# Performance work log

Hardware: AMD Instinct MI355X
Metric: run time of the kernel (lower is better)

## Reference

```python
import jax, jax.numpy as jnp
import numpy as np

HID = 1024
HEADS = 16
HEAD_DIM = HID // HEADS
FFN = 4096
EPS = 1e-5


def setup_inputs() -> dict:
    key = jax.random.key(0)
    ks = jax.random.split(key, 12)
    s = lambda k, shape, fan_in: jax.random.normal(k, shape, jnp.float32) * (fan_in ** -0.5)
    return {
        "hidden_states": jax.random.normal(ks[0], (2, 2048, HID), jnp.float32),
        "Wq": s(ks[1], (HID, HID), HID),
        "Wk": s(ks[2], (HID, HID), HID),
        "Wv": s(ks[3], (HID, HID), HID),
        "Wo": s(ks[4], (HID, HID), HID),
        "W1": s(ks[5], (HID, FFN), HID),
        "b1": jnp.zeros((FFN,), jnp.float32),
        "W2": s(ks[6], (FFN, HID), FFN),
        "b2": jnp.zeros((HID,), jnp.float32),
        "ln1_scale": jnp.ones((HID,), jnp.float32),
        "ln1_shift": jnp.zeros((HID,), jnp.float32),
        "ln2_scale": jnp.ones((HID,), jnp.float32),
        "ln2_shift": jnp.zeros((HID,), jnp.float32),
    }


def _layer_norm(x, scale, shift):
    mean = jnp.mean(x, axis=-1, keepdims=True)
    var = jnp.var(x, axis=-1, keepdims=True)  # biased, matches unbiased=False
    return (x - mean) * jax.lax.rsqrt(var + EPS) * scale + shift


def _forward(hidden_states, Wq, Wk, Wv, Wo, W1, b1, W2, b2,
             ln1_scale, ln1_shift, ln2_scale, ln2_shift):
    bsz, seq_len, _ = hidden_states.shape
    residual = hidden_states
    x = _layer_norm(hidden_states, ln1_scale, ln1_shift)

    # q/k/v projections -> [b, h, s, d]
    def proj(W):
        return (x @ W).reshape(bsz, seq_len, HEADS, HEAD_DIM).transpose(0, 2, 1, 3)
    q, k, v = proj(Wq), proj(Wk), proj(Wv)

    scores = jnp.einsum("bhqd,bhkd->bhqk", q, k)
    causal = jnp.triu(jnp.ones((seq_len, seq_len), bool), k=1)
    scores = jnp.where(causal, -jnp.inf, scores) / (HEAD_DIM ** 0.5)
    attn = jax.nn.softmax(scores, axis=-1)  # dropout is identity in eval
    out = jnp.einsum("bhqk,bhkd->bhqd", attn, v)
    out = out.transpose(0, 2, 1, 3).reshape(bsz, seq_len, HID)
    hidden_states = residual + out @ Wo

    residual = hidden_states
    y = _layer_norm(hidden_states, ln2_scale, ln2_shift)
    y = jax.nn.gelu(y @ W1 + b1, approximate=False) @ W2 + b2  # torch nn.GELU default = exact erf
    return residual + y


def reference(hidden_states, Wq, Wk, Wv, Wo, W1, b1, W2, b2,
              ln1_scale, ln1_shift, ln2_scale, ln2_shift):
    return _forward(hidden_states, Wq, Wk, Wv, Wo, W1, b1, W2, b2,
                    ln1_scale, ln1_shift, ln2_scale, ln2_shift)
```

## Files before the change

kernel.cpp:

```cpp
#include <hip/hip_runtime.h>
#include <math.h>

using bf16x8 = __attribute__((ext_vector_type(8))) short;
using f32x4  = __attribute__((ext_vector_type(4))) float;

struct __align__(8) us4 { unsigned short x, y, z, w; };

__device__ __forceinline__ unsigned short f2b(float f) {
  union { float f; unsigned u; } v; v.f = f;
  unsigned r = v.u + 0x7FFFu + ((v.u >> 16) & 1u);
  return (unsigned short)(r >> 16);
}

#define GLDS(g, l) __builtin_amdgcn_global_load_lds(                        \
    (const __attribute__((address_space(1))) void*)(g),                    \
    (__attribute__((address_space(3))) void*)(l), 16, 0, 0)

__global__ void __launch_bounds__(256) transpose_w(
    const float* __restrict__ src, unsigned short* __restrict__ dst,
    int K, int N) {
  __shared__ float tile[32][33];
  const int n0 = blockIdx.x * 32, k0 = blockIdx.y * 32;
  const int tx = threadIdx.x & 31, ty = threadIdx.x >> 5;
#pragma unroll
  for (int i = 0; i < 32; i += 8)
    tile[ty + i][tx] = src[(size_t)(k0 + ty + i) * N + n0 + tx];
  __syncthreads();
#pragma unroll
  for (int i = 0; i < 32; i += 8)
    dst[(size_t)(n0 + ty + i) * K + k0 + tx] = f2b(tile[tx][ty + i]);
}

__global__ void __launch_bounds__(256) ln_kernel(
    const float* __restrict__ in, const float* __restrict__ scale,
    const float* __restrict__ shift, unsigned short* __restrict__ out) {
  const int row = blockIdx.x, t = threadIdx.x;
  const float4 v = ((const float4*)(in + (size_t)row * 1024))[t];
  float s  = v.x + v.y + v.z + v.w;
  float s2 = v.x * v.x + v.y * v.y + v.z * v.z + v.w * v.w;
#pragma unroll
  for (int off = 32; off; off >>= 1) {
    s  += __shfl_xor(s,  off);
    s2 += __shfl_xor(s2, off);
  }
  __shared__ float red[8];
  const int w = t >> 6, lane = t & 63;
  if (!lane) { red[w] = s; red[4 + w] = s2; }
  __syncthreads();
  s  = red[0] + red[1] + red[2] + red[3];
  s2 = red[4] + red[5] + red[6] + red[7];
  const float mean = s * (1.0f / 1024.0f);
  const float var  = s2 * (1.0f / 1024.0f) - mean * mean;
  const float rstd = rsqrtf(var + 1e-5f);
  const float4 sc = ((const float4*)scale)[t];
  const float4 sh = ((const float4*)shift)[t];
  us4 o;
  o.x = f2b((v.x - mean) * rstd * sc.x + sh.x);
  o.y = f2b((v.y - mean) * rstd * sc.y + sh.y);
  o.z = f2b((v.z - mean) * rstd * sc.z + sh.z);
  o.w = f2b((v.w - mean) * rstd * sc.w + sh.w);
  ((us4*)(out + (size_t)row * 1024))[t] = o;
}

template <int MODE, int BM>
__global__ void __launch_bounds__(256) gemm_bt(
    const unsigned short* __restrict__ A, const unsigned short* __restrict__ B,
    int K, int N,
    float* __restrict__ outf, unsigned short* __restrict__ outb,
    const float* __restrict__ bias, const float* __restrict__ resid,
    unsigned short* __restrict__ vt) {
  constexpr int WN = (BM == 128) ? 2 : 4;
  constexpr int NJ = 128 / (16 * WN);
  constexpr int ACH = BM / 32;
  __shared__ unsigned short lA[2][BM * 64];
  __shared__ unsigned short lB[2][128 * 64];
  const int t = threadIdx.x, lane = t & 63;
  const int w = t >> 6, wm = w / WN, wn = w % WN;
  const int r16 = lane & 15, g = lane >> 4;
  const int m0 = blockIdx.x * BM, n0 = blockIdx.y * 128;

  const unsigned short* aSrc[ACH];
  const unsigned short* bSrc[4];
#pragma unroll
  for (int p = 0; p < ACH; ++p) {
    const int ci = t + p * 256, m = ci >> 3, cs = ci & 7;
    aSrc[p] = A + (size_t)(m0 + m) * K + (cs ^ (m & 7)) * 8;
  }
#pragma unroll
  for (int p = 0; p < 4; ++p) {
    const int ci = t + p * 256, m = ci >> 3, cs = ci & 7;
    bSrc[p] = B + (size_t)(n0 + m) * K + (cs ^ (m & 7)) * 8;
  }

  int aOff[4][2], bOff[NJ][2];
#pragma unroll
  for (int i = 0; i < 4; ++i)
#pragma unroll
    for (int ks = 0; ks < 2; ++ks) {
      const int m = wm * 64 + i * 16 + r16, kb = ks * 4 + g;
      aOff[i][ks] = ((m << 3) + (kb ^ (m & 7))) << 3;
    }
#pragma unroll
  for (int j = 0; j < NJ; ++j)
#pragma unroll
    for (int ks = 0; ks < 2; ++ks) {
      const int n = wn * (16 * NJ) + j * 16 + r16, kb = ks * 4 + g;
      bOff[j][ks] = ((n << 3) + (kb ^ (n & 7))) << 3;
    }

  auto stage = [&](int buf, int kt) {
    const int off = kt * 64;
#pragma unroll
    for (int p = 0; p < ACH; ++p)
      GLDS(aSrc[p] + off, &lA[buf][(t + p * 256) * 8]);
#pragma unroll
    for (int p = 0; p < 4; ++p)
      GLDS(bSrc[p] + off, &lB[buf][(t + p * 256) * 8]);
  };

  f32x4 acc[4][NJ] = {};
  const int nkt = K >> 6;
  stage(0, 0);
  __syncthreads();
  for (int kt = 0; kt < nkt; ++kt) {
    const int cur = kt & 1;
    if (kt + 1 < nkt) stage(cur ^ 1, kt + 1);
    const unsigned short* bA = lA[cur];
    const unsigned short* bB = lB[cur];
#pragma unroll
    for (int ks = 0; ks < 2; ++ks) {
      bf16x8 af[4], bfr[NJ];
#pragma unroll
      for (int i = 0; i < 4; ++i) af[i] = *(const bf16x8*)&bA[aOff[i][ks]];
#pragma unroll
      for (int j = 0; j < NJ; ++j) bfr[j] = *(const bf16x8*)&bB[bOff[j][ks]];
#pragma unroll
      for (int i = 0; i < 4; ++i)
#pragma unroll
        for (int j = 0; j < NJ; ++j)
          acc[i][j] = __builtin_amdgcn_mfma_f32_16x16x32_bf16(
              af[i], bfr[j], acc[i][j], 0, 0, 0);
    }
    __syncthreads();
  }

  float bj[NJ];
  if constexpr (MODE == 2 || MODE == 3) {
#pragma unroll
    for (int j = 0; j < NJ; ++j)
      bj[j] = bias[n0 + wn * (16 * NJ) + j * 16 + r16];
  }
#pragma unroll
  for (int i = 0; i < 4; ++i) {
    const int row0 = m0 + wm * 64 + i * 16 + g * 4;
#pragma unroll
    for (int j = 0; j < NJ; ++j) {
      const int colb = n0 + wn * (16 * NJ) + j * 16;
      const int col = colb + r16;
      if constexpr (MODE == 0) {
        if (colb < 2048) {
#pragma unroll
          for (int r = 0; r < 4; ++r)
            outb[(size_t)(row0 + r) * 2048 + col] = f2b(acc[i][j][r]);
        } else {
          const int b = row0 >> 11, s0 = row0 & 2047;
          us4 pk;
          pk.x = f2b(acc[i][j][0]); pk.y = f2b(acc[i][j][1]);
          pk.z = f2b(acc[i][j][2]); pk.w = f2b(acc[i][j][3]);
          *(us4*)&vt[((size_t)b * 1024 + (col - 2048)) * 2048 + s0] = pk;
        }
      } else if constexpr (MODE == 1) {
#pragma unroll
        for (int r = 0; r < 4; ++r) {
          const size_t idx = (size_t)(row0 + r) * N + col;
          outf[idx] = acc[i][j][r] + resid[idx];
        }
      } else if constexpr (MODE == 2) {
#pragma unroll
        for (int r = 0; r < 4; ++r) {
          const float x = acc[i][j][r] + bj[j];
          const float u = x * (0.7978845608028654f + 0.03567740814f * x * x);
          const float e = __builtin_amdgcn_exp2f(u * 2.885390081777927f);
          const float th = 1.0f - 2.0f * __builtin_amdgcn_rcpf(e + 1.0f);
          outb[(size_t)(row0 + r) * N + col] = f2b(0.5f * x * (1.0f + th));
        }
      } else {
#pragma unroll
        for (int r = 0; r < 4; ++r) {
          const size_t idx = (size_t)(row0 + r) * N + col;
          outf[idx] = acc[i][j][r] + bj[j] + resid[idx];
        }
      }
    }
  }
}

__global__ void __launch_bounds__(256) attn_kernel(
    const unsigned short* __restrict__ qk, const unsigned short* __restrict__ vt,
    unsigned short* __restrict__ obuf) {
  const int j = blockIdx.x, h = blockIdx.y, bb = blockIdx.z;
  const int t = threadIdx.x, lane = t & 63, w = t >> 6;
  const int r16 = lane & 15, g = lane >> 4;
  __shared__ unsigned short lK[2][64 * 64];
  __shared__ unsigned short lV[2][64 * 64];
  __shared__ unsigned short lP[4][16 * 72];

  const int qtA = j, qtB = 31 - j;
  const int ktmax = qtB;
  const int qrowA = qtA * 64 + w * 16 + r16;
  const int qrowB = qtB * 64 + w * 16 + r16;
  const float CE = 0.18033688011112042f;

  bf16x8 qfA[2], qfB[2];
  {
    const unsigned short* qa =
        qk + (size_t)(bb * 2048 + qrowA) * 2048 + h * 64;
    qfA[0] = *(const bf16x8*)(qa + g * 8);
    qfA[1] = *(const bf16x8*)(qa + 32 + g * 8);
    const unsigned short* qb =
        qk + (size_t)(bb * 2048 + qrowB) * 2048 + h * 64;
    qfB[0] = *(const bf16x8*)(qb + g * 8);
    qfB[1] = *(const bf16x8*)(qb + 32 + g * 8);
  }

  f32x4 accA[4] = {}, accB[4] = {};
  float mA = -3.0e38f, lA_ = 0.0f, mB = -3.0e38f, lB_ = 0.0f;

  auto stage = [&](int buf, int kt) {
    const int k0 = kt * 64;
#pragma unroll
    for (int p = 0; p < 2; ++p) {
      const int ci = t + p * 256;
      const int r = ci >> 3, cs = ci & 7;
      const int cb = cs ^ (r & 7);
      GLDS(qk + (size_t)(bb * 2048 + k0 + r) * 2048 + 1024 + h * 64 + cb * 8,
           &lK[buf][ci * 8]);
      GLDS(vt + ((size_t)bb * 1024 + h * 64 + r) * 2048 + k0 + cb * 8,
           &lV[buf][ci * 8]);
    }
  };

  auto flash_step = [&](const bf16x8* qf, f32x4* accO, float& mrun,
                        float& lrun, int qrow, bool diag, int k0, int cur) {
    f32x4 s[4] = {};
#pragma unroll
    for (int ks = 0; ks < 2; ++ks)
#pragma unroll
      for (int mt = 0; mt < 4; ++mt) {
        const int r = mt * 16 + r16, db = ks * 4 + g;
        const bf16x8 kf =
            *(const bf16x8*)&lK[cur][((r << 3) + (db ^ (r & 7))) << 3];
        s[mt] = __builtin_amdgcn_mfma_f32_16x16x32_bf16(kf, qf[ks], s[mt],
                                                        0, 0, 0);
      }
    if (diag) {
#pragma unroll
      for (int mt = 0; mt < 4; ++mt)
#pragma unroll
        for (int r = 0; r < 4; ++r)
          if (k0 + mt * 16 + g * 4 + r > qrow) s[mt][r] = -3.0e38f;
    }
    float tmax = -3.0e38f;
#pragma unroll
    for (int mt = 0; mt < 4; ++mt)
#pragma unroll
      for (int r = 0; r < 4; ++r) tmax = fmaxf(tmax, s[mt][r]);
    tmax = fmaxf(tmax, __shfl_xor(tmax, 16));
    tmax = fmaxf(tmax, __shfl_xor(tmax, 32));
    const float mnew = fmaxf(mrun, tmax);
    const float fac = __builtin_amdgcn_exp2f((mrun - mnew) * CE);
    float pv[4][4];
    float tsum = 0.0f;
#pragma unroll
    for (int mt = 0; mt < 4; ++mt)
#pragma unroll
      for (int r = 0; r < 4; ++r) {
        pv[mt][r] = __builtin_amdgcn_exp2f((s[mt][r] - mnew) * CE);
        tsum += pv[mt][r];
      }
    tsum += __shfl_xor(tsum, 16);
    tsum += __shfl_xor(tsum, 32);
    lrun = lrun * fac + tsum;
    mrun = mnew;
#pragma unroll
    for (int mt = 0; mt < 4; ++mt) {
      us4 pk;
      pk.x = f2b(pv[mt][0]); pk.y = f2b(pv[mt][1]);
      pk.z = f2b(pv[mt][2]); pk.w = f2b(pv[mt][3]);
      *(us4*)&lP[w][r16 * 72 + mt * 16 + g * 4] = pk;
    }
    float fr[4];
#pragma unroll
    for (int r = 0; r < 4; ++r) fr[r] = __shfl(fac, g * 4 + r);
#pragma unroll
    for (int nb = 0; nb < 4; ++nb)
#pragma unroll
      for (int r = 0; r < 4; ++r) accO[nb][r] *= fr[r];
#pragma unroll
    for (int ks = 0; ks < 2; ++ks) {
      const bf16x8 pa = *(const bf16x8*)&lP[w][r16 * 72 + ks * 32 + g * 8];
#pragma unroll
      for (int nb = 0; nb < 4; ++nb) {
        const int d = nb * 16 + r16, kb = ks * 4 + g;
        const bf16x8 vf =
            *(const bf16x8*)&lV[cur][((d << 3) + (kb ^ (d & 7))) << 3];
        accO[nb] = __builtin_amdgcn_mfma_f32_16x16x32_bf16(pa, vf, accO[nb],
                                                           0, 0, 0);
      }
    }
  };

  stage(0, 0);
  __syncthreads();
  int cur = 0;
  for (int kt = 0; kt <= ktmax; ++kt) {
    if (kt < ktmax) stage(cur ^ 1, kt + 1);
    flash_step(qfB, accB, mB, lB_, qrowB, kt == qtB, kt * 64, cur);
    if (kt <= qtA)
      flash_step(qfA, accA, mA, lA_, qrowA, kt == qtA, kt * 64, cur);
    __syncthreads();
    cur ^= 1;
  }

  auto epilogue = [&](const f32x4* accO, float lrun, int q0) {
    const float li = 1.0f / lrun;
    float lr_[4];
#pragma unroll
    for (int r = 0; r < 4; ++r) lr_[r] = __shfl(li, g * 4 + r);
#pragma unroll
    for (int nb = 0; nb < 4; ++nb)
#pragma unroll
      for (int r = 0; r < 4; ++r) {
        const int row = bb * 2048 + q0 + w * 16 + g * 4 + r;
        const int col = h * 64 + nb * 16 + r16;
        obuf[(size_t)row * 1024 + col] = f2b(accO[nb][r] * lr_[r]);
      }
  };
  epilogue(accA, lA_, qtA * 64);
  epilogue(accB, lB_, qtB * 64);
}

extern "C" void kernel_launch(void* const* d_in, const int* in_sizes, int n_in,
                              void* d_out, int out_size, void* d_ws,
                              size_t ws_size, hipStream_t stream) {
  const float* hs   = (const float*)d_in[0];
  const float* Wq   = (const float*)d_in[1];
  const float* Wk   = (const float*)d_in[2];
  const float* Wv   = (const float*)d_in[3];
  const float* Wo   = (const float*)d_in[4];
  const float* W1   = (const float*)d_in[5];
  const float* b1   = (const float*)d_in[6];
  const float* W2   = (const float*)d_in[7];
  const float* b2   = (const float*)d_in[8];
  const float* ln1s = (const float*)d_in[9];
  const float* ln1b = (const float*)d_in[10];
  const float* ln2s = (const float*)d_in[11];
  const float* ln2b = (const float*)d_in[12];
  float* out = (float*)d_out;

  char* ws = (char*)d_ws;
  unsigned short* wqkvT = (unsigned short*)(ws + 0);
  unsigned short* woT   = (unsigned short*)(ws + 6291456);
  unsigned short* w1T   = (unsigned short*)(ws + 8388608);
  unsigned short* w2T   = (unsigned short*)(ws + 16777216);
  float*          hid   = (float*)(ws + 25165824);
  unsigned short* xb    = (unsigned short*)(ws + 41943040);
  char*           big   = ws + 50331648;
  unsigned short* qkb   = (unsigned short*)(big);
  unsigned short* vtb   = (unsigned short*)(big + 16777216);
  unsigned short* ob    = (unsigned short*)(big + 25165824);
  unsigned short* h1    = (unsigned short*)(big);

  transpose_w<<<dim3(32, 32), 256, 0, stream>>>(Wq, wqkvT, 1024, 1024);
  transpose_w<<<dim3(32, 32), 256, 0, stream>>>(Wk, wqkvT + 1024 * 1024, 1024, 1024);
  transpose_w<<<dim3(32, 32), 256, 0, stream>>>(Wv, wqkvT + 2 * 1024 * 1024, 1024, 1024);
  transpose_w<<<dim3(32, 32), 256, 0, stream>>>(Wo, woT, 1024, 1024);
  transpose_w<<<dim3(128, 32), 256, 0, stream>>>(W1, w1T, 1024, 4096);
  transpose_w<<<dim3(32, 128), 256, 0, stream>>>(W2, w2T, 4096, 1024);

  ln_kernel<<<4096, 256, 0, stream>>>(hs, ln1s, ln1b, xb);
  gemm_bt<0, 128><<<dim3(32, 24), 256, 0, stream>>>(xb, wqkvT, 1024, 3072,
                                                    nullptr, qkb, nullptr, nullptr, vtb);
  attn_kernel<<<dim3(16, 16, 2), 256, 0, stream>>>(qkb, vtb, ob);
  gemm_bt<1, 64><<<dim3(64, 8), 256, 0, stream>>>(ob, woT, 1024, 1024,
                                                  hid, nullptr, nullptr, hs, nullptr);
  ln_kernel<<<4096, 256, 0, stream>>>(hid, ln2s, ln2b, xb);
  gemm_bt<2, 128><<<dim3(32, 32), 256, 0, stream>>>(xb, w1T, 1024, 4096,
                                                    nullptr, h1, b1, nullptr, nullptr);
  gemm_bt<3, 64><<<dim3(64, 8), 256, 0, stream>>>(h1, w2T, 4096, 1024,
                                                  out, nullptr, b2, hid, nullptr);
}
```

Baseline: 245.1 us.

## Split attention KV range across two blocks and merge partial softmax results

Each attention block's causal KV range is split into two halves, doubling the grid to 1024 blocks. Each half writes unnormalized bf16 partial outputs plus running max and sum, and a new merge kernel combines them with log-sum-exp weights. The aim is better CU occupancy and load balance, since 512 blocks underfill the GPU. It also adds lazy rescaling (skip the rescale when the max barely grows), packed bf16 conversion via v_cvt_pk_bf16_f32, an XOR-swizzled P buffer, and s_setprio around the MFMAs. The costs are an extra launch, extra global traffic for the partials, and some precision loss from storing partials in bf16.

Result: slower. 257.7 us (+5.1%).

```diff
diff --git a/kernel.cpp b/kernel.cpp
--- a/kernel.cpp
+++ b/kernel.cpp
@@ -5,11 +5,21 @@
 using f32x4  = __attribute__((ext_vector_type(4))) float;
 
 struct __align__(8) us4 { unsigned short x, y, z, w; };
+struct __align__(8) u32x2 { unsigned int x, y; };
 
 __device__ __forceinline__ unsigned short f2b(float f) {
   union { float f; unsigned u; } v; v.f = f;
   unsigned r = v.u + 0x7FFFu + ((v.u >> 16) & 1u);
   return (unsigned short)(r >> 16);
+}
+__device__ __forceinline__ float b2f(unsigned short b) {
+  union { unsigned u; float f; } v; v.u = ((unsigned)b) << 16;
+  return v.f;
+}
+__device__ __forceinline__ unsigned int cvt_pk_bf16(float lo, float hi) {
+  unsigned int d;
+  asm("v_cvt_pk_bf16_f32 %0, %1, %2" : "=v"(d) : "v"(lo), "v"(hi));
+  return d;
 }
 
 #define GLDS(g, l) __builtin_amdgcn_global_load_lds(                        \
@@ -197,28 +207,33 @@
 
 __global__ void __launch_bounds__(256) attn_kernel(
     const unsigned short* __restrict__ qk, const unsigned short* __restrict__ vt,
-    unsigned short* __restrict__ obuf) {
-  const int j = blockIdx.x, h = blockIdx.y, bb = blockIdx.z;
+    unsigned short* __restrict__ Op, float* __restrict__ mlm,
+    float* __restrict__ mll) {
+  const int j = blockIdx.x, h = blockIdx.y;
+  const int bb = blockIdx.z >> 1, half = blockIdx.z & 1;
   const int t = threadIdx.x, lane = t & 63, w = t >> 6;
   const int r16 = lane & 15, g = lane >> 4;
   __shared__ unsigned short lK[2][64 * 64];
   __shared__ unsigned short lV[2][64 * 64];
-  __shared__ unsigned short lP[4][16 * 72];
+  __shared__ unsigned short lP[4][16 * 64];
 
   const int qtA = j, qtB = 31 - j;
-  const int ktmax = qtB;
+  const int ca = (j + 2) >> 1;
+  const int cb = (33 - j) >> 1;
+  const int alo = half ? ca : 0, ahi = half ? (qtA + 1) : ca;
+  const int blo = half ? cb : 0, bhi = half ? (qtB + 1) : cb;
+  const int start = (alo < ahi) ? min(alo, blo) : blo;
+  const int kend = bhi;
   const int qrowA = qtA * 64 + w * 16 + r16;
   const int qrowB = qtB * 64 + w * 16 + r16;
   const float CE = 0.18033688011112042f;
 
   bf16x8 qfA[2], qfB[2];
   {
-    const unsigned short* qa =
-        qk + (size_t)(bb * 2048 + qrowA) * 2048 + h * 64;
+    const unsigned short* qa = qk + (size_t)(bb * 2048 + qrowA) * 2048 + h * 64;
     qfA[0] = *(const bf16x8*)(qa + g * 8);
     qfA[1] = *(const bf16x8*)(qa + 32 + g * 8);
-    const unsigned short* qb =
-        qk + (size_t)(bb * 2048 + qrowB) * 2048 + h * 64;
+    const unsigned short* qb = qk + (size_t)(bb * 2048 + qrowB) * 2048 + h * 64;
     qfB[0] = *(const bf16x8*)(qb + g * 8);
     qfB[1] = *(const bf16x8*)(qb + 32 + g * 8);
   }
@@ -232,17 +247,20 @@
     for (int p = 0; p < 2; ++p) {
       const int ci = t + p * 256;
       const int r = ci >> 3, cs = ci & 7;
-      const int cb = cs ^ (r & 7);
-      GLDS(qk + (size_t)(bb * 2048 + k0 + r) * 2048 + 1024 + h * 64 + cb * 8,
+      const int cb2 = cs ^ (r & 7);
+      GLDS(qk + (size_t)(bb * 2048 + k0 + r) * 2048 + 1024 + h * 64 + cb2 * 8,
            &lK[buf][ci * 8]);
-      GLDS(vt + ((size_t)bb * 1024 + h * 64 + r) * 2048 + k0 + cb * 8,
+      GLDS(vt + ((size_t)bb * 1024 + h * 64 + r) * 2048 + k0 + cb2 * 8,
            &lV[buf][ci * 8]);
     }
   };
+
+  const int pswz = (r16 & 7) << 3;
 
   auto flash_step = [&](const bf16x8* qf, f32x4* accO, float& mrun,
                         float& lrun, int qrow, bool diag, int k0, int cur) {
     f32x4 s[4] = {};
+    __builtin_amdgcn_s_setprio(1);
 #pragma unroll
     for (int ks = 0; ks < 2; ++ks)
 #pragma unroll
@@ -253,6 +271,7 @@
         s[mt] = __builtin_amdgcn_mfma_f32_16x16x32_bf16(kf, qf[ks], s[mt],
                                                         0, 0, 0);
       }
+    __builtin_amdgcn_s_setprio(0);
     if (diag) {
 #pragma unroll
       for (int mt = 0; mt < 4; ++mt)
@@ -267,38 +286,43 @@
       for (int r = 0; r < 4; ++r) tmax = fmaxf(tmax, s[mt][r]);
     tmax = fmaxf(tmax, __shfl_xor(tmax, 16));
     tmax = fmaxf(tmax, __shfl_xor(tmax, 32));
-    const float mnew = fmaxf(mrun, tmax);
-    const float fac = __builtin_amdgcn_exp2f((mrun - mnew) * CE);
+    if (!__all(tmax <= mrun + 44.0f)) {
+      const float mnew = fmaxf(mrun, tmax);
+      const float fac = __builtin_amdgcn_exp2f((mrun - mnew) * CE);
+      lrun *= fac;
+      float fr[4];
+#pragma unroll
+      for (int r = 0; r < 4; ++r) fr[r] = __shfl(fac, g * 4 + r);
+#pragma unroll
+      for (int nb = 0; nb < 4; ++nb)
+#pragma unroll
+        for (int r = 0; r < 4; ++r) accO[nb][r] *= fr[r];
+      mrun = mnew;
+    }
     float pv[4][4];
     float tsum = 0.0f;
 #pragma unroll
     for (int mt = 0; mt < 4; ++mt)
 #pragma unroll
       for (int r = 0; r < 4; ++r) {
-        pv[mt][r] = __builtin_amdgcn_exp2f((s[mt][r] - mnew) * CE);
+        pv[mt][r] = __builtin_amdgcn_exp2f((s[mt][r] - mrun) * CE);
         tsum += pv[mt][r];
       }
     tsum += __shfl_xor(tsum, 16);
     tsum += __shfl_xor(tsum, 32);
-    lrun = lrun * fac + tsum;
-    mrun = mnew;
+    lrun += tsum;
 #pragma unroll
     for (int mt = 0; mt < 4; ++mt) {
-      us4 pk;
-      pk.x = f2b(pv[mt][0]); pk.y = f2b(pv[mt][1]);
-      pk.z = f2b(pv[mt][2]); pk.w = f2b(pv[mt][3]);
-      *(us4*)&lP[w][r16 * 72 + mt * 16 + g * 4] = pk;
-    }
-    float fr[4];
-#pragma unroll
-    for (int r = 0; r < 4; ++r) fr[r] = __shfl(fac, g * 4 + r);
-#pragma unroll
-    for (int nb = 0; nb < 4; ++nb)
-#pragma unroll
-      for (int r = 0; r < 4; ++r) accO[nb][r] *= fr[r];
+      u32x2 pk;
+      pk.x = cvt_pk_bf16(pv[mt][0], pv[mt][1]);
+      pk.y = cvt_pk_bf16(pv[mt][2], pv[mt][3]);
+      *(u32x2*)&lP[w][r16 * 64 + ((mt * 16 + g * 4) ^ pswz)] = pk;
+    }
+    __builtin_amdgcn_s_setprio(1);
 #pragma unroll
     for (int ks = 0; ks < 2; ++ks) {
-      const bf16x8 pa = *(const bf16x8*)&lP[w][r16 * 72 + ks * 32 + g * 8];
+      const bf16x8 pa =
+          *(const bf16x8*)&lP[w][r16 * 64 + ((ks * 32 + g * 8) ^ pswz)];
 #pragma unroll
       for (int nb = 0; nb < 4; ++nb) {
         const int d = nb * 16 + r16, kb = ks * 4 + g;
@@ -308,36 +332,63 @@
                                                            0, 0, 0);
       }
     }
+    __builtin_amdgcn_s_setprio(0);
   };
 
-  stage(0, 0);
+  stage(0, start);
   __syncthreads();
   int cur = 0;
-  for (int kt = 0; kt <= ktmax; ++kt) {
-    if (kt < ktmax) stage(cur ^ 1, kt + 1);
-    flash_step(qfB, accB, mB, lB_, qrowB, kt == qtB, kt * 64, cur);
-    if (kt <= qtA)
+  for (int kt = start; kt < kend; ++kt) {
+    if (kt + 1 < kend) stage(cur ^ 1, kt + 1);
+    if (kt >= blo)
+      flash_step(qfB, accB, mB, lB_, qrowB, kt == qtB, kt * 64, cur);
+    if (kt >= alo && kt < ahi)
       flash_step(qfA, accA, mA, lA_, qrowA, kt == qtA, kt * 64, cur);
     __syncthreads();
     cur ^= 1;
   }
 
-  auto epilogue = [&](const f32x4* accO, float lrun, int q0) {
-    const float li = 1.0f / lrun;
-    float lr_[4];
-#pragma unroll
-    for (int r = 0; r < 4; ++r) lr_[r] = __shfl(li, g * 4 + r);
+  const int Rbase = (bb * 16 + h) * 2048;
+  auto epi = [&](const f32x4* accO, float mrun, float lrun, int q0) {
 #pragma unroll
     for (int nb = 0; nb < 4; ++nb)
 #pragma unroll
       for (int r = 0; r < 4; ++r) {
-        const int row = bb * 2048 + q0 + w * 16 + g * 4 + r;
-        const int col = h * 64 + nb * 16 + r16;
-        obuf[(size_t)row * 1024 + col] = f2b(accO[nb][r] * lr_[r]);
+        const int q = q0 + w * 16 + g * 4 + r;
+        Op[((size_t)half * 65536 + Rbase + q) * 64 + nb * 16 + r16] =
+            f2b(accO[nb][r]);
       }
+    if (g == 0) {
+      const int q = q0 + w * 16 + r16;
+      mlm[half * 65536 + Rbase + q] = mrun;
+      mll[half * 65536 + Rbase + q] = lrun;
+    }
   };
-  epilogue(accA, lA_, qtA * 64);
-  epilogue(accB, lB_, qtB * 64);
+  epi(accA, mA, lA_, qtA * 64);
+  epi(accB, mB, lB_, qtB * 64);
+}
+
+__global__ void __launch_bounds__(256) attn_merge(
+    const unsigned short* __restrict__ Op, const float* __restrict__ mlm,
+    const float* __restrict__ mll, unsigned short* __restrict__ obuf) {
+  const int R = blockIdx.x * 16 + (threadIdx.x >> 4);
+  const int c = (threadIdx.x & 15) * 4;
+  const float CE = 0.18033688011112042f;
+  const float m0 = mlm[R], m1 = mlm[65536 + R];
+  const float l0 = mll[R], l1 = mll[65536 + R];
+  const float m = fmaxf(m0, m1);
+  const float w0 = __builtin_amdgcn_exp2f((m0 - m) * CE);
+  const float w1 = __builtin_amdgcn_exp2f((m1 - m) * CE);
+  const float inv = 1.0f / (l0 * w0 + l1 * w1);
+  const us4 a = *(const us4*)&Op[(size_t)R * 64 + c];
+  const us4 b = *(const us4*)&Op[((size_t)65536 + R) * 64 + c];
+  us4 o;
+  o.x = f2b((b2f(a.x) * w0 + b2f(b.x) * w1) * inv);
+  o.y = f2b((b2f(a.y) * w0 + b2f(b.y) * w1) * inv);
+  o.z = f2b((b2f(a.z) * w0 + b2f(b.z) * w1) * inv);
+  o.w = f2b((b2f(a.w) * w0 + b2f(b.w) * w1) * inv);
+  const int bb = R >> 15, h = (R >> 11) & 15, q = R & 2047;
+  *(us4*)&obuf[(size_t)(bb * 2048 + q) * 1024 + h * 64 + c] = o;
 }
 
 extern "C" void kernel_launch(void* const* d_in, const int* in_sizes, int n_in,
@@ -370,6 +421,10 @@
   unsigned short* vtb   = (unsigned short*)(big + 16777216);
   unsigned short* ob    = (unsigned short*)(big + 25165824);
   unsigned short* h1    = (unsigned short*)(big);
+  char*           att   = ws + 83886080;
+  unsigned short* OpB   = (unsigned short*)(att);
+  float*          mlmB  = (float*)(att + 16777216);
+  float*          mllB  = (float*)(att + 17301504);
 
   transpose_w<<<dim3(32, 32), 256, 0, stream>>>(Wq, wqkvT, 1024, 1024);
   transpose_w<<<dim3(32, 32), 256, 0, stream>>>(Wk, wqkvT + 1024 * 1024, 1024, 1024);
@@ -381,7 +436,8 @@
   ln_kernel<<<4096, 256, 0, stream>>>(hs, ln1s, ln1b, xb);
   gemm_bt<0, 128><<<dim3(32, 24), 256, 0, stream>>>(xb, wqkvT, 1024, 3072,
                                                     nullptr, qkb, nullptr, nullptr, vtb);
-  attn_kernel<<<dim3(16, 16, 2), 256, 0, stream>>>(qkb, vtb, ob);
+  attn_kernel<<<dim3(16, 16, 4), 256, 0, stream>>>(qkb, vtb, OpB, mlmB, mllB);
+  attn_merge<<<4096, 256, 0, stream>>>(OpB, mlmB, mllB, ob);
   gemm_bt<1, 64><<<dim3(64, 8), 256, 0, stream>>>(ob, woT, 1024, 1024,
                                                   hid, nullptr, nullptr, hs, nullptr);
   ln_kernel<<<4096, 256, 0, stream>>>(hid, ln2s, ln2b, xb);
```

## Add 256x256-tile 512-thread GEMM kernel for QKV and FFN1 projections

Applied to the files above, without the earlier changes.

Introduces a new gemm256 kernel with 256x256 output tiles, 8 waves, double-buffered global_load_lds staging and setprio around MFMA bursts. The QKV projection and the FFN1+GELU GEMM now use it, while the smaller-N GEMMs keep the old kernel, which is trimmed to its remaining modes. Larger tiles raise arithmetic intensity and cut redundant operand loads. The cost is far fewer blocks (192 and 256 workgroups on a large-CU GPU), heavier register and LDS pressure (128 KB of LDS per block), and possible under-occupancy.

Measured after the change: 247.0 us. About the same (+0.8%).

```diff
diff --git a/kernel.cpp b/kernel.cpp
--- a/kernel.cpp
+++ b/kernel.cpp
@@ -62,13 +62,130 @@
   ((us4*)(out + (size_t)row * 1024))[t] = o;
 }
 
+template <int MODE>
+__global__ void __launch_bounds__(512, 2) gemm256(
+    const unsigned short* __restrict__ A, const unsigned short* __restrict__ B,
+    int K, int N, unsigned short* __restrict__ outb,
+    const float* __restrict__ bias, unsigned short* __restrict__ vt) {
+  __shared__ unsigned short lA[2][256 * 64];
+  __shared__ unsigned short lB[2][256 * 64];
+  const int t = threadIdx.x, lane = t & 63;
+  const int w = t >> 6, wm = w >> 2, wn = w & 3;
+  const int r16 = lane & 15, g = lane >> 4;
+  const int m0 = blockIdx.x * 256, n0 = blockIdx.y * 256;
+
+  const unsigned short* aSrc[4];
+  const unsigned short* bSrc[4];
+#pragma unroll
+  for (int p = 0; p < 4; ++p) {
+    const int ci = t + p * 512, r = ci >> 3, cs = ci & 7;
+    aSrc[p] = A + (size_t)(m0 + r) * K + (cs ^ (r & 7)) * 8;
+    bSrc[p] = B + (size_t)(n0 + r) * K + (cs ^ (r & 7)) * 8;
+  }
+  int aOff[8][2], bOff[4][2];
+#pragma unroll
+  for (int i = 0; i < 8; ++i)
+#pragma unroll
+    for (int ks = 0; ks < 2; ++ks) {
+      const int m = wm * 128 + i * 16 + r16, kb = ks * 4 + g;
+      aOff[i][ks] = ((m << 3) + (kb ^ (m & 7))) << 3;
+    }
+#pragma unroll
+  for (int j = 0; j < 4; ++j)
+#pragma unroll
+    for (int ks = 0; ks < 2; ++ks) {
+      const int n = wn * 64 + j * 16 + r16, kb = ks * 4 + g;
+      bOff[j][ks] = ((n << 3) + (kb ^ (n & 7))) << 3;
+    }
+
+  auto stage = [&](int buf, int kt) {
+    const int off = kt * 64;
+#pragma unroll
+    for (int p = 0; p < 4; ++p) {
+      GLDS(aSrc[p] + off, &lA[buf][(t + p * 512) * 8]);
+      GLDS(bSrc[p] + off, &lB[buf][(t + p * 512) * 8]);
+    }
+  };
+
+  f32x4 acc[8][4] = {};
+  const int nkt = K >> 6;
+  stage(0, 0);
+  for (int kt = 0; kt < nkt; ++kt) {
+    const int cur = kt & 1;
+    if (kt + 1 < nkt) {
+      stage(cur ^ 1, kt + 1);
+      asm volatile("s_waitcnt vmcnt(8)" ::: "memory");
+    } else {
+      asm volatile("s_waitcnt vmcnt(0)" ::: "memory");
+    }
+    __builtin_amdgcn_s_barrier();
+    __builtin_amdgcn_sched_barrier(0);
+    const unsigned short* bA = lA[cur];
+    const unsigned short* bB = lB[cur];
+#pragma unroll
+    for (int ks = 0; ks < 2; ++ks) {
+      bf16x8 af[8], bfr[4];
+#pragma unroll
+      for (int i = 0; i < 8; ++i) af[i] = *(const bf16x8*)&bA[aOff[i][ks]];
+#pragma unroll
+      for (int j = 0; j < 4; ++j) bfr[j] = *(const bf16x8*)&bB[bOff[j][ks]];
+      __builtin_amdgcn_s_setprio(1);
+#pragma unroll
+      for (int i = 0; i < 8; ++i)
+#pragma unroll
+        for (int j = 0; j < 4; ++j)
+          acc[i][j] = __builtin_amdgcn_mfma_f32_16x16x32_bf16(
+              af[i], bfr[j], acc[i][j], 0, 0, 0);
+      __builtin_amdgcn_s_setprio(0);
+    }
+    __builtin_amdgcn_sched_barrier(0);
+    __builtin_amdgcn_s_barrier();
+  }
+
+  float bj[4];
+  if constexpr (MODE == 2) {
+#pragma unroll
+    for (int j = 0; j < 4; ++j) bj[j] = bias[n0 + wn * 64 + j * 16 + r16];
+  }
+#pragma unroll
+  for (int i = 0; i < 8; ++i) {
+    const int row0 = m0 + wm * 128 + i * 16 + g * 4;
+#pragma unroll
+    for (int j = 0; j < 4; ++j) {
+      const int colb = n0 + wn * 64 + j * 16;
+      const int col = colb + r16;
+      if constexpr (MODE == 0) {
+        if (colb < 2048) {
+#pragma unroll
+          for (int r = 0; r < 4; ++r)
+            outb[(size_t)(row0 + r) * 2048 + col] = f2b(acc[i][j][r]);
+        } else {
+          const int b = row0 >> 11, s0 = row0 & 2047;
+          us4 pk;
+          pk.x = f2b(acc[i][j][0]); pk.y = f2b(acc[i][j][1]);
+          pk.z = f2b(acc[i][j][2]); pk.w = f2b(acc[i][j][3]);
+          *(us4*)&vt[((size_t)b * 1024 + (col - 2048)) * 2048 + s0] = pk;
+        }
+      } else {
+#pragma unroll
+        for (int r = 0; r < 4; ++r) {
+          const float x = acc[i][j][r] + bj[j];
+          const float u = x * (0.7978845608028654f + 0.03567740814f * x * x);
+          const float e = __builtin_amdgcn_exp2f(u * 2.885390081777927f);
+          const float th = 1.0f - 2.0f * __builtin_amdgcn_rcpf(e + 1.0f);
+          outb[(size_t)(row0 + r) * N + col] = f2b(0.5f * x * (1.0f + th));
+        }
+      }
+    }
+  }
+}
+
 template <int MODE, int BM>
 __global__ void __launch_bounds__(256) gemm_bt(
     const unsigned short* __restrict__ A, const unsigned short* __restrict__ B,
     int K, int N,
-    float* __restrict__ outf, unsigned short* __restrict__ outb,
-    const float* __restrict__ bias, const float* __restrict__ resid,
-    unsigned short* __restrict__ vt) {
+    float* __restrict__ outf, const float* __restrict__ bias,
+    const float* __restrict__ resid) {
   constexpr int WN = (BM == 128) ? 2 : 4;
   constexpr int NJ = 128 / (16 * WN);
   constexpr int ACH = BM / 32;
@@ -145,7 +262,7 @@
   }
 
   float bj[NJ];
-  if constexpr (MODE == 2 || MODE == 3) {
+  if constexpr (MODE == 3) {
 #pragma unroll
     for (int j = 0; j < NJ; ++j)
       bj[j] = bias[n0 + wn * (16 * NJ) + j * 16 + r16];
@@ -155,34 +272,12 @@
     const int row0 = m0 + wm * 64 + i * 16 + g * 4;
 #pragma unroll
     for (int j = 0; j < NJ; ++j) {
-      const int colb = n0 + wn * (16 * NJ) + j * 16;
-      const int col = colb + r16;
-      if constexpr (MODE == 0) {
-        if (colb < 2048) {
-#pragma unroll
-          for (int r = 0; r < 4; ++r)
-            outb[(size_t)(row0 + r) * 2048 + col] = f2b(acc[i][j][r]);
-        } else {
-          const int b = row0 >> 11, s0 = row0 & 2047;
-          us4 pk;
-          pk.x = f2b(acc[i][j][0]); pk.y = f2b(acc[i][j][1]);
-          pk.z = f2b(acc[i][j][2]); pk.w = f2b(acc[i][j][3]);
-          *(us4*)&vt[((size_t)b * 1024 + (col - 2048)) * 2048 + s0] = pk;
-        }
-      } else if constexpr (MODE == 1) {
+      const int col = n0 + wn * (16 * NJ) + j * 16 + r16;
+      if constexpr (MODE == 1) {
 #pragma unroll
         for (int r = 0; r < 4; ++r) {
           const size_t idx = (size_t)(row0 + r) * N + col;
           outf[idx] = acc[i][j][r] + resid[idx];
-        }
-      } else if constexpr (MODE == 2) {
-#pragma unroll
-        for (int r = 0; r < 4; ++r) {
-          const float x = acc[i][j][r] + bj[j];
-          const float u = x * (0.7978845608028654f + 0.03567740814f * x * x);
-          const float e = __builtin_amdgcn_exp2f(u * 2.885390081777927f);
-          const float th = 1.0f - 2.0f * __builtin_amdgcn_rcpf(e + 1.0f);
-          outb[(size_t)(row0 + r) * N + col] = f2b(0.5f * x * (1.0f + th));
         }
       } else {
 #pragma unroll
@@ -379,14 +474,14 @@
   transpose_w<<<dim3(32, 128), 256, 0, stream>>>(W2, w2T, 4096, 1024);
 
   ln_kernel<<<4096, 256, 0, stream>>>(hs, ln1s, ln1b, xb);
-  gemm_bt<0, 128><<<dim3(32, 24), 256, 0, stream>>>(xb, wqkvT, 1024, 3072,
-                                                    nullptr, qkb, nullptr, nullptr, vtb);
+  gemm256<0><<<dim3(16, 12), 512, 0, stream>>>(xb, wqkvT, 1024, 3072,
+                                               qkb, nullptr, vtb);
   attn_kernel<<<dim3(16, 16, 2), 256, 0, stream>>>(qkb, vtb, ob);
   gemm_bt<1, 64><<<dim3(64, 8), 256, 0, stream>>>(ob, woT, 1024, 1024,
-                                                  hid, nullptr, nullptr, hs, nullptr);
+                                                  hid, nullptr, hs);
   ln_kernel<<<4096, 256, 0, stream>>>(hid, ln2s, ln2b, xb);
-  gemm_bt<2, 128><<<dim3(32, 32), 256, 0, stream>>>(xb, w1T, 1024, 4096,
-                                                    nullptr, h1, b1, nullptr, nullptr);
+  gemm256<2><<<dim3(16, 16), 512, 0, stream>>>(xb, w1T, 1024, 4096,
+                                               h1, b1, nullptr);
   gemm_bt<3, 64><<<dim3(64, 8), 256, 0, stream>>>(h1, w2T, 4096, 1024,
-                                                  out, nullptr, b2, hid, nullptr);
-}
+                                                  out, b2, hid);
+}
```
